# Performance work log

Hardware: AMD Instinct MI355X
Metric: run time of the kernel (lower is better)

The kernel has to match this reference:

```python
import jax, jax.numpy as jnp
import numpy as np
from jax import lax

B, C, H, W = 32, 384, 56, 56


def setup_inputs() -> dict:
    key = jax.random.key(0)
    k1, k2, k3, k4 = jax.random.split(key, 4)
    x = jax.random.normal(k1, (B, C, H, W), dtype=jnp.float32)
    # positional embedding, trunc_normal(std=0.02) ~ small normal
    pe = 0.02 * jax.random.normal(k2, (1, C, H, 1), dtype=jnp.float32)
    # depthwise conv weight: (out=C, in/groups=1, kH=H, kW=1), PyTorch default init scale
    fan_in = H  # in_channels/groups * kH * kW = 1*H*1
    bound = 1.0 / np.sqrt(fan_in)
    weight = jax.random.uniform(k3, (C, 1, H, 1), dtype=jnp.float32, minval=-bound, maxval=bound)
    bias = jax.random.uniform(k4, (C,), dtype=jnp.float32, minval=-bound, maxval=bound)
    return {"x": x, "pe": pe, "weight": weight, "bias": bias}


def reference(x, pe, weight, bias):
    # PE add
    xp = x + pe  # [B,C,H,W]
    # circular pad along H: concat first H-1 rows at the bottom
    x_cat = jnp.concatenate([xp, xp[:, :, : H - 1, :]], axis=2)  # [B,C,2H-1,W]
    # depthwise conv, kernel (H,1), groups=C -> output [B,C,H,W]
    out = lax.conv_general_dilated(
        x_cat, weight,
        window_strides=(1, 1), padding='VALID',
        dimension_numbers=('NCHW', 'OIHW', 'NCHW'),
        feature_group_count=C,
    )
    return out + bias[None, :, None, None]
```

## Files before the change

### kernel.cpp

```cpp
#include <hip/hip_runtime.h>

#define Cc 384
#define Hh 56
#define Ww 56
#define PLANE (Hh*Ww)
#define NF4 14
#define NBLK 2048
#define NPL 6

typedef short short8 __attribute__((ext_vector_type(8)));
typedef float f32x4  __attribute__((ext_vector_type(4)));
typedef unsigned int u32;
typedef u32 u32x2 __attribute__((ext_vector_type(2)));
struct __align__(16) f4 { float x, y, z, w; };

__device__ __forceinline__ u32 cvtpk_bf16(float a, float b) {
    u32 d; asm("v_cvt_pk_bf16_f32 %0, %1, %2" : "=v"(d) : "v"(a), "v"(b));
    return d;
}
__device__ __forceinline__ int swz(int w) { return (w ^ (w >> 2)) & 7; }

__global__ __launch_bounds__(256) __attribute__((amdgpu_waves_per_eu(4, 4)))
void parc_kernel(const float* __restrict__ x, const float* __restrict__ pe,
                 const float* __restrict__ wgt, const float* __restrict__ bias,
                 float* __restrict__ out)
{
    __shared__ __align__(16) unsigned short Xt16[64 * 64];
    __shared__ __align__(16) float Cb[56 * 60];
    __shared__ unsigned short wt2[2][112];

    const int t   = threadIdx.x;
    const int blk = blockIdx.x;

    const int hg = t / NF4, w4q = t % NF4;
    const int Fq = 56 * hg + w4q;
    const int kw = t >= Hh ? t - Hh : t;
    const int l = t & 63, wvi = t >> 6, l15 = l & 15, g = l >> 4;

    {
        const int w = t >> 2, j = t & 3;
        const int blkz = 7 ^ swz(w);
        *reinterpret_cast<u32*>((char*)Xt16 + 128 * w + 16 * blkz + 4 * j) = 0u;
        const int wz = 56 + (t >> 5);
        *reinterpret_cast<u32*>((char*)Xt16 + 128 * wz + 4 * (t & 31)) = 0u;
    }

    f32x4 v0 = {}, v1 = {}, v2 = {}, v3 = {};
    float p0 = 0.f, p1 = 0.f, p2 = 0.f, p3 = 0.f, wld = 0.f, bz = 0.f;

    #define ISSUE(BC) { \
        const f32x4* __restrict__ xin = reinterpret_cast<const f32x4*>(x) + (size_t)(BC) * (PLANE / 4); \
        const int c_ = (BC) % Cc; \
        const float* __restrict__ pec = pe + c_ * Hh; \
        if (t < 196) { \
            v0 = xin[Fq]; v1 = xin[Fq + 14]; v2 = xin[Fq + 28]; v3 = xin[Fq + 42]; \
            p0 = pec[4 * hg]; p1 = pec[4 * hg + 1]; p2 = pec[4 * hg + 2]; p3 = pec[4 * hg + 3]; \
        } \
        if (t < 112) wld = wgt[c_ * Hh + kw]; \
        bz = bias[c_]; }

    #define SCATTER(PAR) { \
        if (t < 112) wt2[PAR][t] = (unsigned short)(cvtpk_bf16(wld, wld) & 0xffffu); \
        if (t < 196) { \
            const int blkb = hg >> 1, sub8 = 8 * (hg & 1); \
            _Pragma("unroll") \
            for (int q = 0; q < 4; ++q) { \
                const int w = 4 * w4q + q; \
                u32x2 d; \
                d[0] = cvtpk_bf16(v0[q] + p0, v1[q] + p1); \
                d[1] = cvtpk_bf16(v2[q] + p2, v3[q] + p3); \
                *reinterpret_cast<u32x2*>((char*)Xt16 + 128 * w + 16 * (blkb ^ swz(w)) + sub8) = d; \
            } \
        } }

    ISSUE(blk)
    SCATTER(0)
    float bzc = bz;
    __syncthreads();

    for (int it = 0; it < NPL; ++it) {
        const int par = it & 1;
        const int bc_cur = blk + NBLK * it;

        short8 afr[2];
        #pragma unroll
        for (int step = 0; step < 2; ++step) {
            #pragma unroll
            for (int j = 0; j < 8; ++j) {
                int idx = 32 * step + 8 * g + j - 16 * wvi - l15 + 56;
                idx = idx < 0 ? 0 : (idx > 111 ? 111 : idx);
                afr[step][j] = (short)wt2[par][idx];
            }
        }

        if (it + 1 < NPL) { ISSUE(blk + NBLK * (it + 1)) }

        f32x4 acc[4];
        #pragma unroll
        for (int ni = 0; ni < 4; ++ni) acc[ni] = (f32x4){bzc, bzc, bzc, bzc};

        #pragma unroll
        for (int step = 0; step < 2; ++step) {
            #pragma unroll
            for (int ni = 0; ni < 4; ++ni) {
                const int w = 16 * ni + l15;
                const int blk0 = g + 4 * step;
                const short8 bfr = *reinterpret_cast<const short8*>(
                    (char*)Xt16 + 128 * w + 16 * (blk0 ^ swz(w)));
                acc[ni] = __builtin_amdgcn_mfma_f32_16x16x32_bf16(afr[step], bfr, acc[ni], 0, 0, 0);
            }
        }

        #pragma unroll
        for (int ni = 0; ni < 4; ++ni) {
            const int wcol = 16 * ni + l15;
            #pragma unroll
            for (int r = 0; r < 4; ++r) {
                const int h = 16 * wvi + 4 * g + r;
                if (h < Hh && wcol < Ww) Cb[60 * h + wcol] = acc[ni][r];
            }
        }
        __syncthreads();

        f4* __restrict__ op = reinterpret_cast<f4*>(out) + (size_t)bc_cur * (PLANE / 4);
        #define GETST(U) { \
            const int rr = (U) / NF4, ww4 = (U) % NF4; \
            op[(U)] = *reinterpret_cast<const f4*>((char*)Cb + 240 * rr + 16 * ww4); }
        GETST(t)
        GETST(t + 256)
        GETST(t + 512)
        if (t < 16) { GETST(t + 768) }
        #undef GETST

        if (it + 1 < NPL) {
            SCATTER(par ^ 1)
            bzc = bz;
            __syncthreads();
        }
    }
    #undef SCATTER
    #undef ISSUE
}

extern "C" void kernel_launch(void* const* d_in, const int* in_sizes, int n_in,
                              void* d_out, int out_size, void* d_ws, size_t ws_size,
                              hipStream_t stream) {
    const float* x  = (const float*)d_in[0];
    const float* pe = (const float*)d_in[1];
    const float* w  = (const float*)d_in[2];
    const float* b  = (const float*)d_in[3];
    float* out      = (float*)d_out;

    parc_kernel<<<dim3(NBLK), 256, 0, stream>>>(x, pe, w, b, out);
}
```

Baseline: 53.98 us.

## Fix channel per block so weights, PE and bias load once

Blocks are now assigned one channel each and walk 8 batch indices of that channel, so the grid shrinks from 2048 to 1536 blocks. Weight, positional embedding and bias are loaded once per block, and the MFMA A-fragment is built once instead of every iteration. This drops the double-buffered weight array and the per-iteration parameter loads. In exchange each block does more sequential planes with fewer blocks in flight, which may lower latency hiding and change load balance across CUs.

```diff
diff --git a/kernel.cpp b/kernel.cpp
--- a/kernel.cpp
+++ b/kernel.cpp
@@ -5,8 +5,8 @@
 #define Ww 56
 #define PLANE (Hh*Ww)
 #define NF4 14
-#define NBLK 2048
-#define NPL 6
+#define NBLK 1536
+#define NPL 8
 
 typedef short short8 __attribute__((ext_vector_type(8)));
 typedef float f32x4  __attribute__((ext_vector_type(4)));
@@ -27,10 +27,13 @@
 {
     __shared__ __align__(16) unsigned short Xt16[64 * 64];
     __shared__ __align__(16) float Cb[56 * 60];
-    __shared__ unsigned short wt2[2][112];
+    __shared__ unsigned short wt2[112];
 
     const int t   = threadIdx.x;
     const int blk = blockIdx.x;
+    const int c    = blk % Cc;
+    const int bgrp = blk / Cc;
+    const size_t bc0 = (size_t)(bgrp * NPL) * Cc + c;
 
     const int hg = t / NF4, w4q = t % NF4;
     const int Fq = 56 * hg + w4q;
@@ -45,22 +48,23 @@
         *reinterpret_cast<u32*>((char*)Xt16 + 128 * wz + 4 * (t & 31)) = 0u;
     }
 
+    float p0 = 0.f, p1 = 0.f, p2 = 0.f, p3 = 0.f;
+    if (t < 196) {
+        const float* __restrict__ pec = pe + c * Hh;
+        p0 = pec[4 * hg]; p1 = pec[4 * hg + 1]; p2 = pec[4 * hg + 2]; p3 = pec[4 * hg + 3];
+    }
+    const float bz = bias[c];
+    if (t < 112) wt2[t] = (unsigned short)(cvtpk_bf16(wgt[c * Hh + kw], 0.f) & 0xffffu);
+
     f32x4 v0 = {}, v1 = {}, v2 = {}, v3 = {};
-    float p0 = 0.f, p1 = 0.f, p2 = 0.f, p3 = 0.f, wld = 0.f, bz = 0.f;
 
     #define ISSUE(BC) { \
         const f32x4* __restrict__ xin = reinterpret_cast<const f32x4*>(x) + (size_t)(BC) * (PLANE / 4); \
-        const int c_ = (BC) % Cc; \
-        const float* __restrict__ pec = pe + c_ * Hh; \
         if (t < 196) { \
             v0 = xin[Fq]; v1 = xin[Fq + 14]; v2 = xin[Fq + 28]; v3 = xin[Fq + 42]; \
-            p0 = pec[4 * hg]; p1 = pec[4 * hg + 1]; p2 = pec[4 * hg + 2]; p3 = pec[4 * hg + 3]; \
-        } \
-        if (t < 112) wld = wgt[c_ * Hh + kw]; \
-        bz = bias[c_]; }
+        } }
 
-    #define SCATTER(PAR) { \
-        if (t < 112) wt2[PAR][t] = (unsigned short)(cvtpk_bf16(wld, wld) & 0xffffu); \
+    #define SCATTER() { \
         if (t < 196) { \
             const int blkb = hg >> 1, sub8 = 8 * (hg & 1); \
             _Pragma("unroll") \
@@ -73,31 +77,29 @@
             } \
         } }
 
-    ISSUE(blk)
-    SCATTER(0)
-    float bzc = bz;
+    ISSUE(bc0)
+    SCATTER()
     __syncthreads();
 
+    short8 afr[2];
+    #pragma unroll
+    for (int step = 0; step < 2; ++step) {
+        #pragma unroll
+        for (int j = 0; j < 8; ++j) {
+            int idx = 32 * step + 8 * g + j - 16 * wvi - l15 + 56;
+            idx = idx < 0 ? 0 : (idx > 111 ? 111 : idx);
+            afr[step][j] = (short)wt2[idx];
+        }
+    }
+
     for (int it = 0; it < NPL; ++it) {
-        const int par = it & 1;
-        const int bc_cur = blk + NBLK * it;
+        const size_t bc_cur = bc0 + (size_t)it * Cc;
 
-        short8 afr[2];
-        #pragma unroll
-        for (int step = 0; step < 2; ++step) {
-            #pragma unroll
-            for (int j = 0; j < 8; ++j) {
-                int idx = 32 * step + 8 * g + j - 16 * wvi - l15 + 56;
-                idx = idx < 0 ? 0 : (idx > 111 ? 111 : idx);
-                afr[step][j] = (short)wt2[par][idx];
-            }
-        }
-
-        if (it + 1 < NPL) { ISSUE(blk + NBLK * (it + 1)) }
+        if (it + 1 < NPL) { ISSUE(bc0 + (size_t)(it + 1) * Cc) }
 
         f32x4 acc[4];
         #pragma unroll
-        for (int ni = 0; ni < 4; ++ni) acc[ni] = (f32x4){bzc, bzc, bzc, bzc};
+        for (int ni = 0; ni < 4; ++ni) acc[ni] = (f32x4){bz, bz, bz, bz};
 
         #pragma unroll
         for (int step = 0; step < 2; ++step) {
@@ -122,7 +124,7 @@
         }
         __syncthreads();
 
-        f4* __restrict__ op = reinterpret_cast<f4*>(out) + (size_t)bc_cur * (PLANE / 4);
+        f4* __restrict__ op = reinterpret_cast<f4*>(out) + bc_cur * (PLANE / 4);
         #define GETST(U) { \
             const int rr = (U) / NF4, ww4 = (U) % NF4; \
             op[(U)] = *reinterpret_cast<const f4*>((char*)Cb + 240 * rr + 16 * ww4); }
@@ -133,8 +135,7 @@
         #undef GETST
 
         if (it + 1 < NPL) {
-            SCATTER(par ^ 1)
-            bzc = bz;
+            SCATTER()
             __syncthreads();
         }
     }
```

Result: slower. 55.95 us (+3.6%).
